# Kernel optimization log

Hardware: AMD Instinct MI355X
Metric: run time of the kernel (lower is better)

## Reference

```python
import jax, jax.numpy as jnp
import numpy as np

H = 1024      # hidden_size
NH = 16       # num_attention_heads
HD = H // NH  # attention_head_size = 64
B, S = 2, 2048


def setup_inputs() -> dict:
    key = jax.random.key(0)
    ks = jax.random.split(key, 8)
    scale = 1.0 / np.sqrt(H)
    return {
        "hidden_states": jax.random.normal(ks[0], (B, S, H), dtype=jnp.float32),
        "attention_mask": jnp.zeros((B, 1, 1, S), dtype=jnp.float32),
        "Wq": jax.random.normal(ks[1], (H, H), dtype=jnp.float32) * scale,
        "bq": jax.random.normal(ks[2], (H,), dtype=jnp.float32) * 0.02,
        "Wk": jax.random.normal(ks[3], (H, H), dtype=jnp.float32) * scale,
        "bk": jax.random.normal(ks[4], (H,), dtype=jnp.float32) * 0.02,
        "Wv": jax.random.normal(ks[5], (H, H), dtype=jnp.float32) * scale,
        "bv": jax.random.normal(ks[6], (H,), dtype=jnp.float32) * 0.02,
    }


def _split_heads(x):
    # [B,S,H] -> [B,NH,S,HD]
    b, s, _ = x.shape
    return x.reshape(b, s, NH, HD).transpose(0, 2, 1, 3)


def reference(hidden_states, attention_mask, Wq, bq, Wk, bk, Wv, bv):
    q = _split_heads(hidden_states @ Wq.T + bq)  # [B,NH,S,HD]
    k = _split_heads(hidden_states @ Wk.T + bk)
    v = _split_heads(hidden_states @ Wv.T + bv)
    scores = jnp.einsum("bhqd,bhkd->bhqk", q, k) / np.sqrt(HD).astype(np.float32)
    scores = scores + attention_mask  # additive mask, broadcast over heads/queries
    weights = jax.nn.softmax(scores, axis=-1)  # dropout is identity in eval mode
    ctx = jnp.einsum("bhqk,bhkd->bhqd", weights, v)  # [B,NH,S,HD]
    return ctx.transpose(0, 2, 1, 3).reshape(hidden_states.shape[0], hidden_states.shape[1], H)
```

## Files before the change

### kernel.cpp

```cpp
#include <hip/hip_runtime.h>
#include <hip/hip_bf16.h>
#include <math.h>

#define HSZ   1024
#define NHEAD 16
#define HDIM  64
#define BATCH 2
#define SEQ   2048

#define LOG2E 1.4426950408889634f

typedef __attribute__((ext_vector_type(8))) short short8;
typedef __attribute__((ext_vector_type(4))) short short4_t;
typedef __attribute__((ext_vector_type(4))) float floatx4;

typedef __attribute__((address_space(1))) const unsigned int gu32;
typedef __attribute__((address_space(3))) unsigned int lu32;

__device__ __forceinline__ void g2lds16(const void* g, void* l) {
    __builtin_amdgcn_global_load_lds((gu32*)g, (lu32*)l, 16, 0, 0);
}

__device__ __forceinline__ short f2bf(float f) {
    union { float f; unsigned u; } v; v.f = f;
    unsigned r = (v.u + 0x7FFF + ((v.u >> 16) & 1)) >> 16;
    return (short)r;
}

__device__ __forceinline__ unsigned pk2(float a, float b) {
    __hip_bfloat162 h = __float22bfloat162_rn(make_float2(a, b));
    return *(unsigned*)&h;
}

__device__ __forceinline__ float ex2(float x) {
#if __has_builtin(__builtin_amdgcn_exp2f)
    return __builtin_amdgcn_exp2f(x);
#else
    return exp2f(x);
#endif
}

__global__ __launch_bounds__(256) void convert_kernel(
    const float4* __restrict__ X, const float4* __restrict__ Wq,
    const float4* __restrict__ Wk, const float4* __restrict__ Wv,
    const float4* __restrict__ Mask,
    short4_t* __restrict__ Xb, short4_t* __restrict__ Wb,
    float4* __restrict__ Mw)
{
    int idx = blockIdx.x * 256 + threadIdx.x;
    if (idx >= 1835008) {
        int t = idx - 1835008;
        float4 f = Mask[t];
        float4 o;
        o.x = f.x * LOG2E; o.y = f.y * LOG2E;
        o.z = f.z * LOG2E; o.w = f.w * LOG2E;
        Mw[t] = o;
        return;
    }
    const float4* src; short4_t* dst;
    if (idx < 1048576) { src = X + idx; dst = Xb + idx; }
    else {
        int t = idx - 1048576;
        int sel = t >> 18;
        int wi  = t & 0x3FFFF;
        src = (sel == 0 ? Wq : sel == 1 ? Wk : Wv) + wi;
        dst = Wb + (sel << 18) + wi;
    }
    float4 f = *src;
    short4_t o;
    o.x = f2bf(f.x); o.y = f2bf(f.y); o.z = f2bf(f.z); o.w = f2bf(f.w);
    *dst = o;
}

__global__ __launch_bounds__(256, 3) void qkv_mfma_kernel(
    const short* __restrict__ Xb, const short* __restrict__ Wb,
    const float* __restrict__ bq, const float* __restrict__ bk,
    const float* __restrict__ bv,
    short* __restrict__ qo, short* __restrict__ ko, short* __restrict__ vT)
{
    __shared__ short Sm[128 * 132];
    short* As = Sm;
    short* Bs = Sm + 8192;

    const int tid  = threadIdx.x;
    const int lane = tid & 63;
    const int w    = tid >> 6;
    const int l    = lane & 15, quad = lane >> 4;
    const int gM   = blockIdx.y * 128;
    const int gN   = blockIdx.x * 128;
    const int wm   = (w >> 1) * 64, wn = (w & 1) * 64;
    const int ci   = lane >> 3, pb = lane & 7;

    floatx4 acc[4][4] = {};

    for (int kt = 0; kt < HSZ / 64; ++kt) {
        const int k0 = kt * 64;
        __syncthreads();
        #pragma unroll
        for (int u = 0; u < 4; ++u) {
            int c  = w * 4 + u;
            int r  = c * 8 + ci;
            int lb = pb ^ (r & 7);
            g2lds16(Xb + (size_t)(gM + r) * HSZ + k0 + lb * 8, &As[c * 512]);
            g2lds16(Wb + (size_t)(gN + r) * HSZ + k0 + lb * 8, &Bs[c * 512]);
        }
        __syncthreads();
        #pragma unroll
        for (int kk = 0; kk < 2; ++kk) {
            short8 a[4], b[4];
            #pragma unroll
            for (int i = 0; i < 4; ++i) {
                int m = wm + i * 16 + l;
                a[i] = *(const short8*)&As[m * 64 + (((quad + kk * 4) ^ (m & 7)) << 3)];
                int n = wn + i * 16 + l;
                b[i] = *(const short8*)&Bs[n * 64 + (((quad + kk * 4) ^ (n & 7)) << 3)];
            }
            #pragma unroll
            for (int i = 0; i < 4; ++i)
                #pragma unroll
                for (int j = 0; j < 4; ++j)
                    acc[i][j] = __builtin_amdgcn_mfma_f32_16x16x32_bf16(
                        a[i], b[j], acc[i][j], 0, 0, 0);
        }
    }

    const int mat = gN >> 10;

    if (mat == 2) {
        __syncthreads();
        #pragma unroll
        for (int j = 0; j < 4; ++j) {
            int fl = wn + j * 16 + l;
            float bv_ = bv[(gN & 1023) + fl];
            #pragma unroll
            for (int i = 0; i < 4; ++i)
                #pragma unroll
                for (int r = 0; r < 4; ++r)
                    Sm[fl * 132 + wm + i * 16 + quad * 4 + r]
                        = f2bf(acc[i][j][r] + bv_);
        }
        __syncthreads();
        const int bb = gM >> 11, ss0 = gM & (SEQ - 1);
        #pragma unroll
        for (int it = 0; it < 16; ++it) {
            int f = (tid >> 5) + it * 8;
            int c = (tid & 31) * 4;
            short4_t val = *(const short4_t*)&Sm[f * 132 + c];
            int b = (c >> 2) & 15;
            int cp = (c & ~63) | ((((b & 8) | ((b & 3) << 1) | ((b >> 2) & 1))) << 2);
            int nft = (gN & 1023) + f;
            int head = nft >> 6, d = nft & 63;
            *(short4_t*)&vT[(((size_t)(bb * NHEAD + head)) * HDIM + d) * SEQ
                            + ss0 + cp] = val;
        }
        return;
    }

    const float* bias = (mat == 0) ? bq : bk;
    short* dst        = (mat == 0) ? qo : ko;
    const float qscale = (mat == 0) ? 0.125f * LOG2E : 1.0f;

    #pragma unroll
    for (int j = 0; j < 4; ++j) {
        int nft = (gN & 1023) + wn + j * 16 + l;
        float bv_ = bias[nft];
        int head = nft >> 6, d = nft & 63;
        #pragma unroll
        for (int i = 0; i < 4; ++i) {
            #pragma unroll
            for (int r = 0; r < 4; ++r) {
                int gr = gM + wm + i * 16 + quad * 4 + r;
                int bb = gr >> 11, ss = gr & (SEQ - 1);
                float val = (acc[i][j][r] + bv_) * qscale;
                dst[((((size_t)bb * NHEAD + head) * SEQ + ss) << 6) + d] = f2bf(val);
            }
        }
    }
}

__global__ __launch_bounds__(256, 2) void attn_kernel(
    const short* __restrict__ Qg, const short* __restrict__ Kg,
    const short* __restrict__ VTg, const float* __restrict__ maskw,
    float* __restrict__ out)
{
    __shared__ short Qs[128 * 64];
    __shared__ alignas(16) short Ks[2][64 * 64];
    __shared__ alignas(16) short Vt[2][64 * 64];
    __shared__ alignas(16) float Ms[2][64];
    __shared__ alignas(16) float Lx[2][4][64];

    const int tid  = threadIdx.x;
    const int lane = tid & 63;
    const int w    = tid >> 6;
    const int l    = lane & 15, quad = lane >> 4;
    const int idx  = blockIdx.x;
    const int bh   = idx & 31;
    const int qt   = idx >> 5;
    const int batch = bh >> 4, head = bh & 15;
    const int qh = w & 1, kh = w >> 1;
    const int ci = lane >> 3, pb = lane & 7;

    const short* Qb = Qg + ((size_t)bh * SEQ + qt * 128) * HDIM;
    const short* Kb = Kg + (size_t)bh * SEQ * HDIM;
    const short* Vb = VTg + (size_t)bh * HDIM * SEQ;
    const float* mrow = maskw + (size_t)batch * SEQ;

    #pragma unroll
    for (int u = 0; u < 4; ++u) {
        int c = w * 4 + u;
        int r = c * 8 + ci;
        int lb = pb ^ (r & 7);
        g2lds16(Qb + (size_t)r * HDIM + lb * 8, &Qs[c * 512]);
    }
    #pragma unroll
    for (int u = 0; u < 2; ++u) {
        int c = w * 2 + u;
        int r = c * 8 + ci;
        int lb = pb ^ (r & 7);
        g2lds16(Kb + (size_t)r * HDIM + lb * 8, &Ks[0][c * 512]);
        g2lds16(Vb + (size_t)r * SEQ + lb * 8, &Vt[0][c * 512]);
    }
    if (tid < 16) g2lds16(mrow + tid * 4, &Ms[0][0]);
    __syncthreads();

    short8 aq[4][2];
    #pragma unroll
    for (int n = 0; n < 4; ++n)
        #pragma unroll
        for (int kk = 0; kk < 2; ++kk) {
            int m = qh * 64 + n * 16 + l;
            aq[n][kk] = *(const short8*)&Qs[m * 64 + (((quad + kk * 4) ^ (m & 7)) << 3)];
        }

    floatx4 o[4][4] = {};
    float l_i[4] = {0.f, 0.f, 0.f, 0.f};

    for (int kt = 0; kt < SEQ / 64; ++kt) {
        const int cur = kt & 1, nxt = cur ^ 1;
        if (kt + 1 < SEQ / 64) {
            const int r0 = (kt + 1) * 64;
            #pragma unroll
            for (int u = 0; u < 2; ++u) {
                int c = w * 2 + u;
                int r = c * 8 + ci;
                int lb = pb ^ (r & 7);
                g2lds16(Kb + (size_t)(r0 + r) * HDIM + lb * 8, &Ks[nxt][c * 512]);
                g2lds16(Vb + (size_t)r * SEQ + r0 + lb * 8, &Vt[nxt][c * 512]);
            }
            if (tid < 16) g2lds16(mrow + r0 + tid * 4, &Ms[nxt][0]);
        }

        float4 mq[2];
        #pragma unroll
        for (int m = 0; m < 2; ++m)
            mq[m] = *(const float4*)&Ms[cur][kh * 32 + m * 16 + quad * 4];

        floatx4 s[2][4];
        #pragma unroll
        for (int m = 0; m < 2; ++m) {
            floatx4 ini = {mq[m].x, mq[m].y, mq[m].z, mq[m].w};
            #pragma unroll
            for (int n = 0; n < 4; ++n) s[m][n] = ini;
        }
        #pragma unroll
        for (int kk = 0; kk < 2; ++kk) {
            short8 ak[2];
            #pragma unroll
            for (int m = 0; m < 2; ++m) {
                int kr = kh * 32 + m * 16 + l;
                ak[m] = *(const short8*)&Ks[cur][kr * 64 + (((quad + kk * 4) ^ (kr & 7)) << 3)];
            }
            #pragma unroll
            for (int m = 0; m < 2; ++m)
                #pragma unroll
                for (int n = 0; n < 4; ++n)
                    s[m][n] = __builtin_amdgcn_mfma_f32_16x16x32_bf16(
                        ak[m], aq[n][kk], s[m][n], 0, 0, 0);
        }

        #pragma unroll
        for (int n = 0; n < 4; ++n) {
            float rs = 0.f;
            #pragma unroll
            for (int m = 0; m < 2; ++m) {
                s[m][n][0] = ex2(s[m][n][0]);
                s[m][n][1] = ex2(s[m][n][1]);
                s[m][n][2] = ex2(s[m][n][2]);
                s[m][n][3] = ex2(s[m][n][3]);
                rs += (s[m][n][0] + s[m][n][1]) + (s[m][n][2] + s[m][n][3]);
            }
            l_i[n] += rs;
        }

        short8 ap[4];
        #pragma unroll
        for (int n = 0; n < 4; ++n) {
            union { unsigned u[4]; short8 s8; } pu;
            pu.u[0] = pk2(s[0][n][0], s[0][n][1]);
            pu.u[1] = pk2(s[0][n][2], s[0][n][3]);
            pu.u[2] = pk2(s[1][n][0], s[1][n][1]);
            pu.u[3] = pk2(s[1][n][2], s[1][n][3]);
            ap[n] = pu.s8;
        }

        short8 bvf[4];
        #pragma unroll
        for (int nd = 0; nd < 4; ++nd) {
            int d = nd * 16 + l;
            bvf[nd] = *(const short8*)&Vt[cur][d * 64 + (((kh * 4 + quad) ^ (d & 7)) << 3)];
        }
        #pragma unroll
        for (int nq = 0; nq < 4; ++nq)
            #pragma unroll
            for (int nd = 0; nd < 4; ++nd)
                o[nq][nd] = __builtin_amdgcn_mfma_f32_16x16x32_bf16(
                    ap[nq], bvf[nd], o[nq][nd], 0, 0, 0);

        __syncthreads();
    }

    float* reg = (qh == 0) ? (float*)&Ks[0][0] : (float*)&Vt[0][0];
    if (kh == 1) {
        #pragma unroll
        for (int nq = 0; nq < 4; ++nq)
            #pragma unroll
            for (int nd = 0; nd < 4; ++nd)
                *(floatx4*)&reg[((nq * 4 + nd) * 64 + lane) * 4] = o[nq][nd];
        #pragma unroll
        for (int n = 0; n < 4; ++n) Lx[qh][n][lane] = l_i[n];
    }
    __syncthreads();
    if (kh == 0) {
        #pragma unroll
        for (int nq = 0; nq < 4; ++nq)
            #pragma unroll
            for (int nd = 0; nd < 4; ++nd)
                o[nq][nd] += *(const floatx4*)&reg[((nq * 4 + nd) * 64 + lane) * 4];
        #pragma unroll
        for (int n = 0; n < 4; ++n) {
            float t = l_i[n] + Lx[qh][n][lane];
            t += __shfl_xor(t, 16);
            t += __shfl_xor(t, 32);
            l_i[n] = t;
        }
        #pragma unroll
        for (int nq = 0; nq < 4; ++nq) {
            #pragma unroll
            for (int r = 0; r < 4; ++r) {
                float inv = 1.0f / __shfl(l_i[nq], (lane & 48) + quad * 4 + r);
                int qrow = qt * 128 + qh * 64 + nq * 16 + quad * 4 + r;
                #pragma unroll
                for (int nd = 0; nd < 4; ++nd)
                    out[((size_t)batch * SEQ + qrow) * HSZ + head * HDIM + nd * 16 + l]
                        = o[nq][nd][r] * inv;
            }
        }
    }
}

extern "C" void kernel_launch(void* const* d_in, const int* in_sizes, int n_in,
                              void* d_out, int out_size, void* d_ws, size_t ws_size,
                              hipStream_t stream) {
    const float* hs   = (const float*)d_in[0];
    const float* mask = (const float*)d_in[1];
    const float* Wq   = (const float*)d_in[2];
    const float* bq   = (const float*)d_in[3];
    const float* Wk   = (const float*)d_in[4];
    const float* bk   = (const float*)d_in[5];
    const float* Wv   = (const float*)d_in[6];
    const float* bv   = (const float*)d_in[7];
    float* out = (float*)d_out;

    short* Xb = (short*)d_ws;
    short* Wb = Xb + 4194304;
    short* qb = Wb + 3145728;
    short* kb = qb + 4194304;
    short* vT = kb + 4194304;
    float* Mw = (float*)(vT + 4194304);

    convert_kernel<<<7172, 256, 0, stream>>>(
        (const float4*)hs, (const float4*)Wq, (const float4*)Wk, (const float4*)Wv,
        (const float4*)mask, (short4_t*)Xb, (short4_t*)Wb, (float4*)Mw);

    dim3 g2(3 * HSZ / 128, BATCH * SEQ / 128);
    qkv_mfma_kernel<<<g2, 256, 0, stream>>>(Xb, Wb, bq, bk, bv, qb, kb, vT);

    attn_kernel<<<512, 256, 0, stream>>>(qb, kb, vT, Mw, out);
}
```

Baseline: 162.8 us.

## Software-pipeline QK^T of next tile with softmax-PV of current tile

Restructures the attention key loop so that the QK^T MFMAs for tile k+1 are issued alongside the exp/pack and PV MFMAs for tile k. K and V loads are now staggered: K runs one tile ahead of V, with ping-pong buffers and the loop unrolled by two. It also raises wave priority around the MFMA blocks with s_setprio. The aim is to hide softmax latency and LDS waits behind matrix work, at the cost of holding two score register sets, which raises register pressure.

```diff
diff --git a/kernel.cpp b/kernel.cpp
--- a/kernel.cpp
+++ b/kernel.cpp
@@ -218,9 +218,11 @@
         int r = c * 8 + ci;
         int lb = pb ^ (r & 7);
         g2lds16(Kb + (size_t)r * HDIM + lb * 8, &Ks[0][c * 512]);
+        g2lds16(Kb + (size_t)(64 + r) * HDIM + lb * 8, &Ks[1][c * 512]);
         g2lds16(Vb + (size_t)r * SEQ + lb * 8, &Vt[0][c * 512]);
     }
     if (tid < 16) g2lds16(mrow + tid * 4, &Ms[0][0]);
+    if (tid >= 64 && tid < 80) g2lds16(mrow + 64 + (tid - 64) * 4, &Ms[1][0]);
     __syncthreads();
 
     short8 aq[4][2];
@@ -234,28 +236,37 @@
 
     floatx4 o[4][4] = {};
     float l_i[4] = {0.f, 0.f, 0.f, 0.f};
-
-    for (int kt = 0; kt < SEQ / 64; ++kt) {
-        const int cur = kt & 1, nxt = cur ^ 1;
-        if (kt + 1 < SEQ / 64) {
-            const int r0 = (kt + 1) * 64;
+    floatx4 sA[2][4], sB[2][4];
+
+    auto PRE = [&](int tK, short* Kdst, float* Mdst, int tV, short* Vdst) {
+        if (tK < SEQ / 64) {
+            const int r0 = tK * 64;
             #pragma unroll
             for (int u = 0; u < 2; ++u) {
                 int c = w * 2 + u;
                 int r = c * 8 + ci;
                 int lb = pb ^ (r & 7);
-                g2lds16(Kb + (size_t)(r0 + r) * HDIM + lb * 8, &Ks[nxt][c * 512]);
-                g2lds16(Vb + (size_t)r * SEQ + r0 + lb * 8, &Vt[nxt][c * 512]);
-            }
-            if (tid < 16) g2lds16(mrow + r0 + tid * 4, &Ms[nxt][0]);
-        }
-
+                g2lds16(Kb + (size_t)(r0 + r) * HDIM + lb * 8, Kdst + c * 512);
+            }
+            if (tid < 16) g2lds16(mrow + r0 + tid * 4, Mdst);
+        }
+        if (tV < SEQ / 64) {
+            const int c0 = tV * 64;
+            #pragma unroll
+            for (int u = 0; u < 2; ++u) {
+                int c = w * 2 + u;
+                int r = c * 8 + ci;
+                int lb = pb ^ (r & 7);
+                g2lds16(Vb + (size_t)r * SEQ + c0 + lb * 8, Vdst + c * 512);
+            }
+        }
+    };
+
+    auto QKT = [&](floatx4 (&s)[2][4], const short* Kbuf, const float* Mbuf) {
         float4 mq[2];
         #pragma unroll
         for (int m = 0; m < 2; ++m)
-            mq[m] = *(const float4*)&Ms[cur][kh * 32 + m * 16 + quad * 4];
-
-        floatx4 s[2][4];
+            mq[m] = *(const float4*)&Mbuf[kh * 32 + m * 16 + quad * 4];
         #pragma unroll
         for (int m = 0; m < 2; ++m) {
             floatx4 ini = {mq[m].x, mq[m].y, mq[m].z, mq[m].w};
@@ -268,16 +279,26 @@
             #pragma unroll
             for (int m = 0; m < 2; ++m) {
                 int kr = kh * 32 + m * 16 + l;
-                ak[m] = *(const short8*)&Ks[cur][kr * 64 + (((quad + kk * 4) ^ (kr & 7)) << 3)];
-            }
+                ak[m] = *(const short8*)&Kbuf[kr * 64 + (((quad + kk * 4) ^ (kr & 7)) << 3)];
+            }
+            __builtin_amdgcn_s_setprio(1);
             #pragma unroll
             for (int m = 0; m < 2; ++m)
                 #pragma unroll
                 for (int n = 0; n < 4; ++n)
                     s[m][n] = __builtin_amdgcn_mfma_f32_16x16x32_bf16(
                         ak[m], aq[n][kk], s[m][n], 0, 0, 0);
-        }
-
+            __builtin_amdgcn_s_setprio(0);
+        }
+    };
+
+    auto SMPV = [&](floatx4 (&s)[2][4], const short* Vbuf) {
+        short8 bvf[4];
+        #pragma unroll
+        for (int nd = 0; nd < 4; ++nd) {
+            int d = nd * 16 + l;
+            bvf[nd] = *(const short8*)&Vbuf[d * 64 + (((kh * 4 + quad) ^ (d & 7)) << 3)];
+        }
         #pragma unroll
         for (int n = 0; n < 4; ++n) {
             float rs = 0.f;
@@ -291,7 +312,6 @@
             }
             l_i[n] += rs;
         }
-
         short8 ap[4];
         #pragma unroll
         for (int n = 0; n < 4; ++n) {
@@ -302,20 +322,28 @@
             pu.u[3] = pk2(s[1][n][2], s[1][n][3]);
             ap[n] = pu.s8;
         }
-
-        short8 bvf[4];
-        #pragma unroll
-        for (int nd = 0; nd < 4; ++nd) {
-            int d = nd * 16 + l;
-            bvf[nd] = *(const short8*)&Vt[cur][d * 64 + (((kh * 4 + quad) ^ (d & 7)) << 3)];
-        }
+        __builtin_amdgcn_s_setprio(1);
         #pragma unroll
         for (int nq = 0; nq < 4; ++nq)
             #pragma unroll
             for (int nd = 0; nd < 4; ++nd)
                 o[nq][nd] = __builtin_amdgcn_mfma_f32_16x16x32_bf16(
                     ap[nq], bvf[nd], o[nq][nd], 0, 0, 0);
-
+        __builtin_amdgcn_s_setprio(0);
+    };
+
+    QKT(sA, &Ks[0][0], &Ms[0][0]);
+    __syncthreads();
+
+    for (int kt = 0; kt < SEQ / 64; kt += 2) {
+        PRE(kt + 2, &Ks[0][0], &Ms[0][0], kt + 1, &Vt[1][0]);
+        QKT(sB, &Ks[1][0], &Ms[1][0]);
+        SMPV(sA, &Vt[0][0]);
+        __syncthreads();
+        PRE(kt + 3, &Ks[1][0], &Ms[1][0], kt + 2, &Vt[0][0]);
+        if (kt + 2 < SEQ / 64)
+            QKT(sA, &Ks[0][0], &Ms[0][0]);
+        SMPV(sB, &Vt[1][0]);
         __syncthreads();
     }
 
```

Measured after the change: 160.2 us. No clear change (-1.6%).

## Triple-buffer K/V tiles with partial vmcnt waits and preload full mask row

Applied to the files above, without the earlier changes.

Moves the attention K/V pipeline from double to triple buffering. Each iteration prefetches two tiles ahead and waits only for the older loads with s_waitcnt vmcnt(4) before a raw barrier. The whole mask row is loaded into LDS once, V fragment loads are hoisted ahead of the exp/softmax work, and MFMA blocks are wrapped in s_setprio. The aim is to hide global load latency behind compute, at the cost of more LDS (which may reduce occupancy) and a hand-tuned vmcnt count that must match the number of outstanding loads.

```diff
diff --git a/kernel.cpp b/kernel.cpp
--- a/kernel.cpp
+++ b/kernel.cpp
@@ -184,9 +184,9 @@
     float* __restrict__ out)
 {
     __shared__ short Qs[128 * 64];
-    __shared__ alignas(16) short Ks[2][64 * 64];
-    __shared__ alignas(16) short Vt[2][64 * 64];
-    __shared__ alignas(16) float Ms[2][64];
+    __shared__ alignas(16) short Ks[3][64 * 64];
+    __shared__ alignas(16) short Vt[3][64 * 64];
+    __shared__ alignas(16) float Mf[SEQ];
     __shared__ alignas(16) float Lx[2][4][64];
 
     const int tid  = threadIdx.x;
@@ -218,9 +218,11 @@
         int r = c * 8 + ci;
         int lb = pb ^ (r & 7);
         g2lds16(Kb + (size_t)r * HDIM + lb * 8, &Ks[0][c * 512]);
+        g2lds16(Kb + (size_t)(64 + r) * HDIM + lb * 8, &Ks[1][c * 512]);
         g2lds16(Vb + (size_t)r * SEQ + lb * 8, &Vt[0][c * 512]);
-    }
-    if (tid < 16) g2lds16(mrow + tid * 4, &Ms[0][0]);
+        g2lds16(Vb + (size_t)r * SEQ + 64 + lb * 8, &Vt[1][c * 512]);
+        g2lds16(mrow + c * 256 + lane * 4, &Mf[c * 256]);
+    }
     __syncthreads();
 
     short8 aq[4][2];
@@ -235,25 +237,24 @@
     floatx4 o[4][4] = {};
     float l_i[4] = {0.f, 0.f, 0.f, 0.f};
 
-    for (int kt = 0; kt < SEQ / 64; ++kt) {
-        const int cur = kt & 1, nxt = cur ^ 1;
-        if (kt + 1 < SEQ / 64) {
-            const int r0 = (kt + 1) * 64;
-            #pragma unroll
-            for (int u = 0; u < 2; ++u) {
-                int c = w * 2 + u;
-                int r = c * 8 + ci;
-                int lb = pb ^ (r & 7);
-                g2lds16(Kb + (size_t)(r0 + r) * HDIM + lb * 8, &Ks[nxt][c * 512]);
-                g2lds16(Vb + (size_t)r * SEQ + r0 + lb * 8, &Vt[nxt][c * 512]);
-            }
-            if (tid < 16) g2lds16(mrow + r0 + tid * 4, &Ms[nxt][0]);
-        }
-
+    auto PRE = [&](int t2) {
+        const int nx = t2 % 3;
+        const int r0 = t2 * 64;
+        #pragma unroll
+        for (int u = 0; u < 2; ++u) {
+            int c = w * 2 + u;
+            int r = c * 8 + ci;
+            int lb = pb ^ (r & 7);
+            g2lds16(Kb + (size_t)(r0 + r) * HDIM + lb * 8, &Ks[nx][c * 512]);
+            g2lds16(Vb + (size_t)r * SEQ + r0 + lb * 8, &Vt[nx][c * 512]);
+        }
+    };
+
+    auto TILE = [&](int kt, const short* kbuf, const short* vbuf) {
         float4 mq[2];
         #pragma unroll
         for (int m = 0; m < 2; ++m)
-            mq[m] = *(const float4*)&Ms[cur][kh * 32 + m * 16 + quad * 4];
+            mq[m] = *(const float4*)&Mf[kt * 64 + kh * 32 + m * 16 + quad * 4];
 
         floatx4 s[2][4];
         #pragma unroll
@@ -268,16 +269,24 @@
             #pragma unroll
             for (int m = 0; m < 2; ++m) {
                 int kr = kh * 32 + m * 16 + l;
-                ak[m] = *(const short8*)&Ks[cur][kr * 64 + (((quad + kk * 4) ^ (kr & 7)) << 3)];
+                ak[m] = *(const short8*)&kbuf[kr * 64 + (((quad + kk * 4) ^ (kr & 7)) << 3)];
             }
+            __builtin_amdgcn_s_setprio(1);
             #pragma unroll
             for (int m = 0; m < 2; ++m)
                 #pragma unroll
                 for (int n = 0; n < 4; ++n)
                     s[m][n] = __builtin_amdgcn_mfma_f32_16x16x32_bf16(
                         ak[m], aq[n][kk], s[m][n], 0, 0, 0);
-        }
-
+            __builtin_amdgcn_s_setprio(0);
+        }
+
+        short8 bvf[4];
+        #pragma unroll
+        for (int nd = 0; nd < 4; ++nd) {
+            int d = nd * 16 + l;
+            bvf[nd] = *(const short8*)&vbuf[d * 64 + (((kh * 4 + quad) ^ (d & 7)) << 3)];
+        }
         #pragma unroll
         for (int n = 0; n < 4; ++n) {
             float rs = 0.f;
@@ -291,7 +300,6 @@
             }
             l_i[n] += rs;
         }
-
         short8 ap[4];
         #pragma unroll
         for (int n = 0; n < 4; ++n) {
@@ -302,20 +310,24 @@
             pu.u[3] = pk2(s[1][n][2], s[1][n][3]);
             ap[n] = pu.s8;
         }
-
-        short8 bvf[4];
-        #pragma unroll
-        for (int nd = 0; nd < 4; ++nd) {
-            int d = nd * 16 + l;
-            bvf[nd] = *(const short8*)&Vt[cur][d * 64 + (((kh * 4 + quad) ^ (d & 7)) << 3)];
-        }
+        __builtin_amdgcn_s_setprio(1);
         #pragma unroll
         for (int nq = 0; nq < 4; ++nq)
             #pragma unroll
             for (int nd = 0; nd < 4; ++nd)
                 o[nq][nd] = __builtin_amdgcn_mfma_f32_16x16x32_bf16(
                     ap[nq], bvf[nd], o[nq][nd], 0, 0, 0);
-
+        __builtin_amdgcn_s_setprio(0);
+    };
+
+    for (int kt = 0; kt < SEQ / 64 - 2; ++kt) {
+        PRE(kt + 2);
+        TILE(kt, &Ks[kt % 3][0], &Vt[kt % 3][0]);
+        asm volatile("s_waitcnt vmcnt(4)" ::: "memory");
+        __builtin_amdgcn_s_barrier();
+    }
+    for (int kt = SEQ / 64 - 2; kt < SEQ / 64; ++kt) {
+        TILE(kt, &Ks[kt % 3][0], &Vt[kt % 3][0]);
         __syncthreads();
     }
 
```

Result: no change. 165.9 us (+1.9%).

## Split attention work across four waves over key tiles with smaller query tiles

Applied to the files above, without the earlier changes.

The attention kernel now processes 64 query rows per block instead of 128 and launches twice as many blocks. All four waves share the same queries and each handles a different 32-key slice of a 128-key step, so the partial outputs and row sums of four waves are reduced through LDS at the end. The double-buffered prefetch is replaced by a load-then-sync scheme per 128-key step, mask values are read directly from global memory, and MFMA sections are raised in priority with s_setprio. The intent is higher occupancy (launch bounds 4) and more blocks to fill the GPU, at the cost of losing load/compute overlap, extra barriers, and a longer cross-wave reduction.

```diff
diff --git a/kernel.cpp b/kernel.cpp
--- a/kernel.cpp
+++ b/kernel.cpp
@@ -178,16 +178,14 @@
     }
 }
 
-__global__ __launch_bounds__(256, 2) void attn_kernel(
+__global__ __launch_bounds__(256, 4) void attn_kernel(
     const short* __restrict__ Qg, const short* __restrict__ Kg,
     const short* __restrict__ VTg, const float* __restrict__ maskw,
     float* __restrict__ out)
 {
-    __shared__ short Qs[128 * 64];
+    __shared__ short Qs[64 * 64];
     __shared__ alignas(16) short Ks[2][64 * 64];
     __shared__ alignas(16) short Vt[2][64 * 64];
-    __shared__ alignas(16) float Ms[2][64];
-    __shared__ alignas(16) float Lx[2][4][64];
 
     const int tid  = threadIdx.x;
     const int lane = tid & 63;
@@ -197,30 +195,21 @@
     const int bh   = idx & 31;
     const int qt   = idx >> 5;
     const int batch = bh >> 4, head = bh & 15;
-    const int qh = w & 1, kh = w >> 1;
+    const int pp = w & 1, kh = w >> 1;
     const int ci = lane >> 3, pb = lane & 7;
 
-    const short* Qb = Qg + ((size_t)bh * SEQ + qt * 128) * HDIM;
+    const short* Qb = Qg + ((size_t)bh * SEQ + qt * 64) * HDIM;
     const short* Kb = Kg + (size_t)bh * SEQ * HDIM;
     const short* Vb = VTg + (size_t)bh * HDIM * SEQ;
     const float* mrow = maskw + (size_t)batch * SEQ;
 
-    #pragma unroll
-    for (int u = 0; u < 4; ++u) {
-        int c = w * 4 + u;
-        int r = c * 8 + ci;
-        int lb = pb ^ (r & 7);
-        g2lds16(Qb + (size_t)r * HDIM + lb * 8, &Qs[c * 512]);
-    }
     #pragma unroll
     for (int u = 0; u < 2; ++u) {
         int c = w * 2 + u;
         int r = c * 8 + ci;
         int lb = pb ^ (r & 7);
-        g2lds16(Kb + (size_t)r * HDIM + lb * 8, &Ks[0][c * 512]);
-        g2lds16(Vb + (size_t)r * SEQ + lb * 8, &Vt[0][c * 512]);
-    }
-    if (tid < 16) g2lds16(mrow + tid * 4, &Ms[0][0]);
+        g2lds16(Qb + (size_t)r * HDIM + lb * 8, &Qs[c * 512]);
+    }
     __syncthreads();
 
     short8 aq[4][2];
@@ -228,39 +217,40 @@
     for (int n = 0; n < 4; ++n)
         #pragma unroll
         for (int kk = 0; kk < 2; ++kk) {
-            int m = qh * 64 + n * 16 + l;
+            int m = n * 16 + l;
             aq[n][kk] = *(const short8*)&Qs[m * 64 + (((quad + kk * 4) ^ (m & 7)) << 3)];
         }
 
     floatx4 o[4][4] = {};
     float l_i[4] = {0.f, 0.f, 0.f, 0.f};
 
-    for (int kt = 0; kt < SEQ / 64; ++kt) {
-        const int cur = kt & 1, nxt = cur ^ 1;
-        if (kt + 1 < SEQ / 64) {
-            const int r0 = (kt + 1) * 64;
-            #pragma unroll
-            for (int u = 0; u < 2; ++u) {
-                int c = w * 2 + u;
-                int r = c * 8 + ci;
-                int lb = pb ^ (r & 7);
-                g2lds16(Kb + (size_t)(r0 + r) * HDIM + lb * 8, &Ks[nxt][c * 512]);
-                g2lds16(Vb + (size_t)r * SEQ + r0 + lb * 8, &Vt[nxt][c * 512]);
-            }
-            if (tid < 16) g2lds16(mrow + r0 + tid * 4, &Ms[nxt][0]);
-        }
-
-        float4 mq[2];
-        #pragma unroll
-        for (int m = 0; m < 2; ++m)
-            mq[m] = *(const float4*)&Ms[cur][kh * 32 + m * 16 + quad * 4];
+    for (int kt = 0; kt < SEQ / 128; ++kt) {
+        __syncthreads();
+        const float* mg = mrow + kt * 128 + pp * 64 + kh * 32;
+        float4 mq0 = *(const float4*)&mg[quad * 4];
+        float4 mq1 = *(const float4*)&mg[16 + quad * 4];
+        #pragma unroll
+        for (int u = 0; u < 2; ++u) {
+            int c = w * 2 + u;
+            int r = c * 8 + ci;
+            int lb = pb ^ (r & 7);
+            size_t kr = (size_t)(kt * 128 + r);
+            g2lds16(Kb + kr * HDIM + lb * 8,                      &Ks[0][c * 512]);
+            g2lds16(Kb + (kr + 64) * HDIM + lb * 8,               &Ks[1][c * 512]);
+            g2lds16(Vb + (size_t)r * SEQ + kt * 128 + lb * 8,      &Vt[0][c * 512]);
+            g2lds16(Vb + (size_t)r * SEQ + kt * 128 + 64 + lb * 8, &Vt[1][c * 512]);
+        }
+        __syncthreads();
+
+        const short* kbuf = &Ks[pp][0];
+        const short* vbuf = &Vt[pp][0];
 
         floatx4 s[2][4];
-        #pragma unroll
-        for (int m = 0; m < 2; ++m) {
-            floatx4 ini = {mq[m].x, mq[m].y, mq[m].z, mq[m].w};
-            #pragma unroll
-            for (int n = 0; n < 4; ++n) s[m][n] = ini;
+        {
+            floatx4 i0 = {mq0.x, mq0.y, mq0.z, mq0.w};
+            floatx4 i1 = {mq1.x, mq1.y, mq1.z, mq1.w};
+            #pragma unroll
+            for (int n = 0; n < 4; ++n) { s[0][n] = i0; s[1][n] = i1; }
         }
         #pragma unroll
         for (int kk = 0; kk < 2; ++kk) {
@@ -268,16 +258,24 @@
             #pragma unroll
             for (int m = 0; m < 2; ++m) {
                 int kr = kh * 32 + m * 16 + l;
-                ak[m] = *(const short8*)&Ks[cur][kr * 64 + (((quad + kk * 4) ^ (kr & 7)) << 3)];
+                ak[m] = *(const short8*)&kbuf[kr * 64 + (((quad + kk * 4) ^ (kr & 7)) << 3)];
             }
+            __builtin_amdgcn_s_setprio(1);
             #pragma unroll
             for (int m = 0; m < 2; ++m)
                 #pragma unroll
                 for (int n = 0; n < 4; ++n)
                     s[m][n] = __builtin_amdgcn_mfma_f32_16x16x32_bf16(
                         ak[m], aq[n][kk], s[m][n], 0, 0, 0);
-        }
-
+            __builtin_amdgcn_s_setprio(0);
+        }
+
+        short8 bvf[4];
+        #pragma unroll
+        for (int nd = 0; nd < 4; ++nd) {
+            int d = nd * 16 + l;
+            bvf[nd] = *(const short8*)&vbuf[d * 64 + (((kh * 4 + quad) ^ (d & 7)) << 3)];
+        }
         #pragma unroll
         for (int n = 0; n < 4; ++n) {
             float rs = 0.f;
@@ -291,7 +289,6 @@
             }
             l_i[n] += rs;
         }
-
         short8 ap[4];
         #pragma unroll
         for (int n = 0; n < 4; ++n) {
@@ -302,43 +299,73 @@
             pu.u[3] = pk2(s[1][n][2], s[1][n][3]);
             ap[n] = pu.s8;
         }
-
-        short8 bvf[4];
-        #pragma unroll
-        for (int nd = 0; nd < 4; ++nd) {
-            int d = nd * 16 + l;
-            bvf[nd] = *(const short8*)&Vt[cur][d * 64 + (((kh * 4 + quad) ^ (d & 7)) << 3)];
-        }
+        __builtin_amdgcn_s_setprio(1);
         #pragma unroll
         for (int nq = 0; nq < 4; ++nq)
             #pragma unroll
             for (int nd = 0; nd < 4; ++nd)
                 o[nq][nd] = __builtin_amdgcn_mfma_f32_16x16x32_bf16(
                     ap[nq], bvf[nd], o[nq][nd], 0, 0, 0);
-
-        __syncthreads();
-    }
-
-    float* reg = (qh == 0) ? (float*)&Ks[0][0] : (float*)&Vt[0][0];
-    if (kh == 1) {
-        #pragma unroll
-        for (int nq = 0; nq < 4; ++nq)
-            #pragma unroll
-            for (int nd = 0; nd < 4; ++nd)
-                *(floatx4*)&reg[((nq * 4 + nd) * 64 + lane) * 4] = o[nq][nd];
-        #pragma unroll
-        for (int n = 0; n < 4; ++n) Lx[qh][n][lane] = l_i[n];
-    }
+        __builtin_amdgcn_s_setprio(0);
+    }
+
+    float* bufA = (float*)&Ks[0][0];
+    float* bufB = (float*)&Vt[0][0];
+    float* Lq   = (float*)&Qs[0];
+
     __syncthreads();
-    if (kh == 0) {
-        #pragma unroll
-        for (int nq = 0; nq < 4; ++nq)
-            #pragma unroll
-            for (int nd = 0; nd < 4; ++nd)
-                o[nq][nd] += *(const floatx4*)&reg[((nq * 4 + nd) * 64 + lane) * 4];
+    if (w == 2) {
+        #pragma unroll
+        for (int nq = 0; nq < 4; ++nq)
+            #pragma unroll
+            for (int nd = 0; nd < 4; ++nd)
+                *(floatx4*)&bufA[((nq * 4 + nd) * 64 + lane) * 4] = o[nq][nd];
+    }
+    if (w == 3) {
+        #pragma unroll
+        for (int nq = 0; nq < 4; ++nq)
+            #pragma unroll
+            for (int nd = 0; nd < 4; ++nd)
+                *(floatx4*)&bufB[((nq * 4 + nd) * 64 + lane) * 4] = o[nq][nd];
+    }
+    if (w >= 1) {
+        #pragma unroll
+        for (int n = 0; n < 4; ++n) Lq[(w - 1) * 256 + n * 64 + lane] = l_i[n];
+    }
+    __syncthreads();
+    if (w == 0) {
+        #pragma unroll
+        for (int nq = 0; nq < 4; ++nq)
+            #pragma unroll
+            for (int nd = 0; nd < 4; ++nd)
+                o[nq][nd] += *(const floatx4*)&bufA[((nq * 4 + nd) * 64 + lane) * 4];
+    }
+    if (w == 1) {
+        #pragma unroll
+        for (int nq = 0; nq < 4; ++nq)
+            #pragma unroll
+            for (int nd = 0; nd < 4; ++nd)
+                o[nq][nd] += *(const floatx4*)&bufB[((nq * 4 + nd) * 64 + lane) * 4];
+    }
+    __syncthreads();
+    if (w == 1) {
+        #pragma unroll
+        for (int nq = 0; nq < 4; ++nq)
+            #pragma unroll
+            for (int nd = 0; nd < 4; ++nd)
+                *(floatx4*)&bufA[((nq * 4 + nd) * 64 + lane) * 4] = o[nq][nd];
+    }
+    __syncthreads();
+    if (w == 0) {
+        #pragma unroll
+        for (int nq = 0; nq < 4; ++nq)
+            #pragma unroll
+            for (int nd = 0; nd < 4; ++nd)
+                o[nq][nd] += *(const floatx4*)&bufA[((nq * 4 + nd) * 64 + lane) * 4];
         #pragma unroll
         for (int n = 0; n < 4; ++n) {
-            float t = l_i[n] + Lx[qh][n][lane];
+            float t = l_i[n] + Lq[n * 64 + lane] + Lq[256 + n * 64 + lane]
+                             + Lq[512 + n * 64 + lane];
             t += __shfl_xor(t, 16);
             t += __shfl_xor(t, 32);
             l_i[n] = t;
@@ -348,7 +375,7 @@
             #pragma unroll
             for (int r = 0; r < 4; ++r) {
                 float inv = 1.0f / __shfl(l_i[nq], (lane & 48) + quad * 4 + r);
-                int qrow = qt * 128 + qh * 64 + nq * 16 + quad * 4 + r;
+                int qrow = qt * 64 + nq * 16 + quad * 4 + r;
                 #pragma unroll
                 for (int nd = 0; nd < 4; ++nd)
                     out[((size_t)batch * SEQ + qrow) * HSZ + head * HDIM + nd * 16 + l]
@@ -385,5 +412,5 @@
     dim3 g2(3 * HSZ / 128, BATCH * SEQ / 128);
     qkv_mfma_kernel<<<g2, 256, 0, stream>>>(Xb, Wb, bq, bk, bv, qb, kb, vT);
 
-    attn_kernel<<<512, 256, 0, stream>>>(qb, kb, vT, Mw, out);
-}
+    attn_kernel<<<1024, 256, 0, stream>>>(qb, kb, vT, Mw, out);
+}
```

New measurement: 363.6 us. 123% more time.
